# Optimization experiments

Hardware: AMD Instinct MI355X
Metric: run time of the kernel (lower is better)

The kernel has to match this reference:

```python
import jax, jax.numpy as jnp
import numpy as np

B, S, D = 1, 2048, 2048
H, KV, HD = 32, 8, 64
POWER = 100000.0


def _rotary(x):
    # x: [B, h, S, HD]; faithful to RotaryEncoder: freqs = pos / div_term
    rot_dim = HD // 2
    pos = jnp.arange(S, dtype=x.dtype)
    div = POWER ** (jnp.arange(0, HD, 2, dtype=x.dtype) / HD)  # [HD//2]
    freqs = pos[:, None] / div  # [S, HD//2]
    cos, sin = jnp.cos(freqs), jnp.sin(freqs)
    x_rot, x_pass = x[..., :rot_dim], x[..., rot_dim:]
    h = rot_dim // 2
    rot_half = jnp.concatenate([-x_rot[..., h:], x_rot[..., :h]], axis=-1)
    return jnp.concatenate([x_rot * cos + rot_half * sin, x_pass], axis=-1)


def setup_inputs() -> dict:
    key = jax.random.key(0)
    k1, k2, k3 = jax.random.split(key, 3)
    hidden_states = jax.random.normal(k1, (B, S, D), dtype=jnp.float32)
    op_size = H * HD + 2 * KV * HD
    Wqkv = jax.random.normal(k2, (D, op_size), dtype=jnp.float32) * 0.02
    Wo = jax.random.normal(k3, (H * HD, D), dtype=jnp.float32) * 0.02
    causal = jnp.tril(jnp.ones((S, S), dtype=bool))
    attention_mask = jnp.where(causal, 0.0, -1e9).astype(jnp.float32)[None, None]
    return {"hidden_states": hidden_states, "attention_mask": attention_mask,
            "Wqkv": Wqkv, "Wo": Wo}


def reference(hidden_states, attention_mask, Wqkv, Wo):
    groups = H // KV
    qkv = hidden_states @ Wqkv  # [B, S, op_size]
    qpos = H * HD
    q = qkv[..., :qpos].reshape(B, S, H, HD).transpose(0, 2, 1, 3)
    k = qkv[..., qpos:qpos + KV * HD].reshape(B, S, KV, HD).transpose(0, 2, 1, 3)
    v = qkv[..., qpos + KV * HD:].reshape(B, S, KV, HD).transpose(0, 2, 1, 3)
    q = _rotary(q)
    k = _rotary(k)
    k = jnp.repeat(k, groups, axis=1)  # GQA repeat_interleave -> [B, H, S, HD]
    v = jnp.repeat(v, groups, axis=1)
    scores = jnp.einsum('bhqd,bhkd->bhqk', q, k) / jnp.sqrt(jnp.float32(HD))
    scores = scores + attention_mask[..., :S]
    attn = jax.nn.softmax(scores.astype(jnp.float32), axis=-1).astype(v.dtype)
    out = jnp.einsum('bhqk,bhkd->bhqd', attn, v)
    out = out.transpose(0, 2, 1, 3).reshape(B, S, H * HD)
    return out @ Wo
```

## Files before the change

### kernel.cpp

```cpp
#include <hip/hip_runtime.h>
#include <hip/hip_bf16.h>
#include <cstdint>
#include <cstddef>

#define S_LEN 2048
#define D_MODEL 2048
#define NH 32
#define NKV 8
#define HDIM 64
#define OPSZ 3072
#define KOFF 2048
#define VOFF 2560

typedef float    floatx4 __attribute__((ext_vector_type(4)));
typedef __bf16   bf16x8  __attribute__((ext_vector_type(8)));
typedef __bf16   bf16x4  __attribute__((ext_vector_type(4)));
typedef __bf16   bf16_t;
typedef _Float16 f16_t;
typedef _Float16 f16x2   __attribute__((ext_vector_type(2)));
typedef _Float16 f16x4   __attribute__((ext_vector_type(4)));
typedef _Float16 f16x8   __attribute__((ext_vector_type(8)));
typedef __fp16   hfx2    __attribute__((ext_vector_type(2)));

__device__ __forceinline__ void gld16(const void* g, void* l) {
  __builtin_amdgcn_global_load_lds((__attribute__((address_space(1))) void*)(void*)g,
                                   (__attribute__((address_space(3))) void*)l,
                                   16, 0, 0);
}

__global__ __launch_bounds__(256)
void prep_kernel(const float* __restrict__ X, const float* __restrict__ Wqkv,
                 const float* __restrict__ Wo, bf16_t* __restrict__ Xb,
                 bf16_t* __restrict__ WqkvT, bf16_t* __restrict__ WoT) {
  const int bx = blockIdx.x;
  const int k0 = blockIdx.y * 32;
  const int tx = threadIdx.x & 31, ty = threadIdx.x >> 5;
  if (bx < 160) {
    __shared__ float tile[32][33];
    const float* W; bf16_t* Wt; int N, n0;
    if (bx < 96) { W = Wqkv; Wt = WqkvT; N = OPSZ;    n0 = bx * 32; }
    else         { W = Wo;   Wt = WoT;   N = D_MODEL; n0 = (bx - 96) * 32; }
#pragma unroll
    for (int i = 0; i < 32; i += 8)
      tile[ty + i][tx] = W[(size_t)(k0 + ty + i) * N + n0 + tx];
    __syncthreads();
#pragma unroll
    for (int i = 0; i < 32; i += 8)
      Wt[(size_t)(n0 + ty + i) * D_MODEL + k0 + tx] = (bf16_t)tile[tx][ty + i];
  } else {
    const int n0 = (bx - 160) * 32;
#pragma unroll
    for (int i = 0; i < 32; i += 8) {
      const size_t idx = (size_t)(k0 + ty + i) * D_MODEL + n0 + tx;
      Xb[idx] = (bf16_t)X[idx];
    }
  }
}

#define GEMM64_CORE(A_, Bt_, K_, m0_, n0_)                                        \
  const int tid = threadIdx.x;                                                    \
  const int wave = tid >> 6;                                                      \
  const int lane = tid & 63;                                                      \
  const int lane15 = lane & 15;                                                   \
  const int quad = lane >> 4;                                                     \
  const int wm = (wave & 1) * 32;                                                 \
  const int wn = (wave >> 1) * 64;                                                \
  floatx4 acc[2][4];                                                              \
  _Pragma("unroll") for (int i = 0; i < 2; i++)                                   \
    _Pragma("unroll") for (int j = 0; j < 4; j++)                                 \
      acc[i][j] = floatx4{0.f, 0.f, 0.f, 0.f};                                    \
  {                                                                               \
     \
    int arow[2], acol[2], apan[2];                                                \
    _Pragma("unroll") for (int i = 0; i < 2; i++) {                               \
      const int c = tid + i * 256;                                                \
      apan[i] = c >> 8; arow[i] = (c & 255) >> 2; acol[i] = (c & 3) * 8;          \
    }                                                                             \
                            \
    int brow[4], bcol[4], bpan[4];                                                \
    _Pragma("unroll") for (int i = 0; i < 4; i++) {                               \
      const int c = tid + i * 256;                                                \
      bpan[i] = c >> 9; brow[i] = (c & 511) >> 2; bcol[i] = (c & 3) * 8;          \
    }                                                                             \
    const bf16_t* Ab = (A_) + (size_t)(m0_) * (K_);                               \
    const bf16_t* Bb = (Bt_) + (size_t)(n0_) * (K_);                              \
    auto stage = [&](bf16_t* dA, bf16_t* dB, int k0) {                            \
      _Pragma("unroll") for (int i = 0; i < 2; i++)                               \
        gld16(Ab + (size_t)arow[i] * (K_) + k0 + apan[i] * 32 + acol[i],          \
              dA + (i * 256 + wave * 64) * 8);                                    \
      _Pragma("unroll") for (int i = 0; i < 4; i++)                               \
        gld16(Bb + (size_t)brow[i] * (K_) + k0 + bpan[i] * 32 + bcol[i],          \
              dB + (i * 256 + wave * 64) * 8);                                    \
    };                                                                            \
    auto comp = [&](const bf16_t* sA, const bf16_t* sB) {                         \
      _Pragma("unroll") for (int kt = 0; kt < 2; kt++) {                          \
        bf16x8 af[2], bfr[4];                                                     \
        _Pragma("unroll") for (int mi = 0; mi < 2; mi++)                          \
          af[mi] = *(const bf16x8*)&sA[kt * 2048 + (wm + mi * 16 + lane15) * 32 + quad * 8]; \
        _Pragma("unroll") for (int ni = 0; ni < 4; ni++)                          \
          bfr[ni] = *(const bf16x8*)&sB[kt * 4096 + (wn + ni * 16 + lane15) * 32 + quad * 8]; \
        _Pragma("unroll") for (int mi = 0; mi < 2; mi++)                          \
          _Pragma("unroll") for (int ni = 0; ni < 4; ni++)                        \
            acc[mi][ni] = __builtin_amdgcn_mfma_f32_16x16x32_bf16(af[mi], bfr[ni],\
                                                                  acc[mi][ni], 0, 0, 0); \
      }                                                                           \
    };                                                                            \
    const int NT = (K_) / 64;                           \
    stage(As0, Bs0, 0);                                                           \
    __syncthreads();                                                              \
    for (int t = 0; t < NT; t += 2) {                                             \
      stage(As1, Bs1, (t + 1) * 64);          \
      comp(As0, Bs0);                                                             \
      __syncthreads();                           \
      if (t + 2 < NT) stage(As0, Bs0, (t + 2) * 64);                              \
      comp(As1, Bs1);                                                             \
      __syncthreads();                                                            \
    }                                                                             \
  }

#define GEMM64_LDS                                                                \
  __shared__ bf16_t As0[2 * 64 * 32];                                             \
  __shared__ bf16_t As1[2 * 64 * 32];                                             \
  __shared__ bf16_t Bs0[2 * 128 * 32];                                            \
  __shared__ bf16_t Bs1[2 * 128 * 32];

#define QSCALE 0.18033688011112042f
__global__ __launch_bounds__(256, 3)
void gemm_qkv_rope(const bf16_t* __restrict__ A, const bf16_t* __restrict__ Bt,
                   bf16_t* __restrict__ Qr, bf16_t* __restrict__ Kr,
                   f16_t* __restrict__ VtG) {
  GEMM64_LDS
  const int m0 = blockIdx.y * 64;
  const int n0 = blockIdx.x * 128;
  GEMM64_CORE(A, Bt, D_MODEL, m0, n0)

  const int colbase = n0 + wn;
  const int s0 = m0 + wm;

  if (colbase < VOFF) {
    const bool isQ = (colbase < KOFF);
    const float k2 = 0.51905126483f;
    const float pj0 = exp2f(-(float)lane15 * k2);
    const float pj1 = pj0 * 0.0031622776601684f;
    bf16_t* dst = isQ ? (Qr + ((size_t)(colbase >> 6) * S_LEN) * HDIM)
                      : (Kr + ((size_t)((colbase - KOFF) >> 6) * S_LEN) * HDIM);
    const float qs = isQ ? QSCALE : 1.0f;
#pragma unroll
    for (int mi = 0; mi < 2; mi++) {
#pragma unroll
      for (int r = 0; r < 4; r++) {
        const int s = s0 + mi * 16 + quad * 4 + r;
        const float sf = (float)s;
        float s0s, s0c, s1s, s1c;
        __sincosf(sf * pj0, &s0s, &s0c);
        __sincosf(sf * pj1, &s1s, &s1c);
        const float x0 = acc[mi][0][r], x1 = acc[mi][1][r];
        bf16_t* row = dst + (size_t)s * HDIM + lane15;
        row[0]  = (bf16_t)((x0 * s0c - x1 * s0s) * qs);
        row[16] = (bf16_t)((x1 * s1c + x0 * s1s) * qs);
        row[32] = (bf16_t)(acc[mi][2][r] * qs);
        row[48] = (bf16_t)(acc[mi][3][r] * qs);
      }
    }
  } else {
    const int kvv = (colbase - VOFF) >> 6;
    f16_t* dst = VtG + (size_t)kvv * HDIM * S_LEN;
#pragma unroll
    for (int mi = 0; mi < 2; mi++) {
      const int s = s0 + mi * 16 + quad * 4;
#pragma unroll
      for (int ni = 0; ni < 4; ni++) {
        const int d = ni * 16 + lane15;
        f16x4 tv;
#pragma unroll
        for (int r = 0; r < 4; r++) tv[r] = (f16_t)acc[mi][ni][r];
        *(f16x4*)&dst[(size_t)d * S_LEN + s] = tv;
      }
    }
  }
}

__global__ __launch_bounds__(256, 3)
void gemm_bt_f32out(const bf16_t* __restrict__ A, const bf16_t* __restrict__ Bt,
                    float* __restrict__ C, int M, int N, int K) {
  GEMM64_LDS
  const int m0 = blockIdx.y * 64;
  const int n0 = blockIdx.x * 128;
  GEMM64_CORE(A, Bt, K, m0, n0)

#pragma unroll
  for (int mi = 0; mi < 2; mi++)
#pragma unroll
    for (int r = 0; r < 4; r++) {
      const int row = m0 + wm + mi * 16 + quad * 4 + r;
#pragma unroll
      for (int ni = 0; ni < 4; ni++) {
        const int col = n0 + wn + ni * 16 + lane15;
        C[(size_t)row * N + col] = acc[mi][ni][r];
      }
    }
}

__global__ __launch_bounds__(256, 4)
void flash_kernel(const bf16_t* __restrict__ Qr, const bf16_t* __restrict__ Kr,
                  const f16_t* __restrict__ VtG, bf16_t* __restrict__ attn) {
  __shared__ bf16_t Ks[128 * 64];
  __shared__ f16_t  Vt[64 * 128];

  const int tid = threadIdx.x;
  const int wave = tid >> 6;
  const int lane = tid & 63;
  const int lane15 = lane & 15;
  const int quad = lane >> 4;
  const int bx = blockIdx.x;
  const int h = bx & 31;
  const int qblk = 31 - (bx >> 5);
  const int q0 = qblk * 64;
  const int rq = q0 + wave * 16;
  const int kv = h >> 2;
  const size_t kbase = (size_t)kv * S_LEN * HDIM;
  const size_t vbase = (size_t)kv * HDIM * S_LEN;

  const int krow0 = tid >> 3;
  const int kcol  = ((((tid & 7) * 16) ^ ((krow0 & 7) << 4)) >> 1);
  const int vd0   = tid >> 4;
  const int vcol  = ((((tid & 15) * 16) ^ ((vd0 & 15) << 4)) >> 1);

  const int kswz = (lane15 & 7) << 4;
  const int vswz = lane15 << 4;

  bf16x8 aq[2];
#pragma unroll
  for (int kt = 0; kt < 2; kt++)
    aq[kt] = *(const bf16x8*)&Qr[((size_t)h * S_LEN + rq + lane15) * HDIM + kt * 32 + quad * 8];

  const f16x4 vone = {(f16_t)1.0f, (f16_t)1.0f, (f16_t)1.0f, (f16_t)1.0f};

  float m_run = -1e30f;
  floatx4 lacc = floatx4{0.f, 0.f, 0.f, 0.f};
  floatx4 o[4];
#pragma unroll
  for (int dt = 0; dt < 4; dt++) o[dt] = floatx4{0.f, 0.f, 0.f, 0.f};

  const int nk = (qblk + 2) >> 1;

  for (int t = 0; t < nk; ++t) {
    const int p0 = t * 128;
    __syncthreads();
#pragma unroll
    for (int i = 0; i < 4; i++)
      gld16(Kr + kbase + (size_t)(p0 + krow0 + i * 32) * HDIM + kcol,
            &Ks[(i * 256 + wave * 64) * 8]);
#pragma unroll
    for (int i = 0; i < 4; i++)
      gld16(VtG + vbase + (size_t)(vd0 + i * 16) * S_LEN + p0 + vcol,
            &Vt[(i * 256 + wave * 64) * 8]);
    __syncthreads();

    floatx4 sc[8];
#pragma unroll
    for (int nt = 0; nt < 8; nt++) sc[nt] = floatx4{0.f, 0.f, 0.f, 0.f};
#pragma unroll
    for (int kt = 0; kt < 2; kt++) {
#pragma unroll
      for (int nt = 0; nt < 8; nt++) {
        const bf16x8 ak = *(const bf16x8*)&Ks[(nt * 16 + lane15) * 64 +
                                              (((kt * 64 + quad * 16) ^ kswz) >> 1)];
        sc[nt] = __builtin_amdgcn_mfma_f32_16x16x32_bf16(ak, aq[kt], sc[nt], 0, 0, 0);
      }
    }

    if (p0 + 127 > rq) {
#pragma unroll
      for (int nt = 0; nt < 8; nt++)
#pragma unroll
        for (int r = 0; r < 4; r++) {
          const int kpos = p0 + nt * 16 + quad * 4 + r;
          const int qrow = rq + lane15;
          if (kpos > qrow) sc[nt][r] = -1e30f;
        }
    }

    float mt = -1e30f;
#pragma unroll
    for (int nt = 0; nt < 8; nt++) {
      mt = fmaxf(fmaxf(mt, sc[nt][0]), sc[nt][1]);
      mt = fmaxf(fmaxf(mt, sc[nt][2]), sc[nt][3]);
    }
    mt = fmaxf(mt, __shfl_xor(mt, 16));
    mt = fmaxf(mt, __shfl_xor(mt, 32));
    const float mnew = fmaxf(m_run, mt);
    const float alpha = __builtin_amdgcn_exp2f(m_run - mnew);
    m_run = mnew;

    f16x4 ph[8];
#pragma unroll
    for (int nt = 0; nt < 8; nt++) {
      const float e0 = __builtin_amdgcn_exp2f(sc[nt][0] - mnew);
      const float e1 = __builtin_amdgcn_exp2f(sc[nt][1] - mnew);
      const float e2 = __builtin_amdgcn_exp2f(sc[nt][2] - mnew);
      const float e3 = __builtin_amdgcn_exp2f(sc[nt][3] - mnew);
      const hfx2 lo_ = __builtin_amdgcn_cvt_pkrtz(e0, e1);
      const hfx2 hi_ = __builtin_amdgcn_cvt_pkrtz(e2, e3);
      const f16x2 lo = __builtin_bit_cast(f16x2, lo_);
      const f16x2 hi = __builtin_bit_cast(f16x2, hi_);
      ph[nt] = __builtin_shufflevector(lo, hi, 0, 1, 2, 3);
    }

    lacc = lacc * alpha;
#pragma unroll
    for (int dt = 0; dt < 4; dt++) o[dt] = o[dt] * alpha;

#pragma unroll
    for (int kt4 = 0; kt4 < 8; kt4++) {
      lacc = __builtin_amdgcn_mfma_f32_16x16x16f16(vone, ph[kt4], lacc, 0, 0, 0);
#pragma unroll
      for (int dt = 0; dt < 4; dt++) {
        const f16x4 av = *(const f16x4*)&Vt[(dt * 16 + lane15) * 128 +
                                            (((kt4 * 32 + quad * 8) ^ vswz) >> 1)];
        o[dt] = __builtin_amdgcn_mfma_f32_16x16x16f16(av, ph[kt4], o[dt], 0, 0, 0);
      }
    }
  }

  const float inv = 1.0f / lacc[0];
  const int s = rq + lane15;
#pragma unroll
  for (int dt = 0; dt < 4; dt++) {
    bf16x4 tv;
#pragma unroll
    for (int r = 0; r < 4; r++) tv[r] = (bf16_t)(o[dt][r] * inv);
    *(bf16x4*)&attn[(size_t)s * D_MODEL + h * HDIM + dt * 16 + quad * 4] = tv;
  }
}

extern "C" void kernel_launch(void* const* d_in, const int* in_sizes, int n_in,
                              void* d_out, int out_size, void* d_ws, size_t ws_size,
                              hipStream_t stream) {
  (void)in_sizes; (void)n_in; (void)out_size; (void)ws_size;
  const float* hidden = (const float*)d_in[0];
  const float* Wqkv = (const float*)d_in[2];
  const float* Wo   = (const float*)d_in[3];
  float* out = (float*)d_out;

  char* ws = (char*)d_ws;
  size_t off = 0;
  auto alloc = [&](size_t bytes) -> void* {
    void* p = ws + off;
    off += (bytes + 255) & ~(size_t)255;
    return p;
  };
  bf16_t* Xb    = (bf16_t*)alloc((size_t)S_LEN * D_MODEL * 2);
  bf16_t* WqkvT = (bf16_t*)alloc((size_t)OPSZ * D_MODEL * 2);
  bf16_t* WoT   = (bf16_t*)alloc((size_t)D_MODEL * D_MODEL * 2);
  bf16_t* Qr    = (bf16_t*)alloc((size_t)NH * S_LEN * HDIM * 2);
  bf16_t* Kr    = (bf16_t*)alloc((size_t)NKV * S_LEN * HDIM * 2);
  f16_t*  VtG   = (f16_t*) alloc((size_t)NKV * HDIM * S_LEN * 2);
  bf16_t* attn  = (bf16_t*)alloc((size_t)S_LEN * D_MODEL * 2);

  prep_kernel<<<dim3(224, 64), 256, 0, stream>>>(hidden, Wqkv, Wo, Xb, WqkvT, WoT);
  gemm_qkv_rope<<<dim3(OPSZ / 128, S_LEN / 64), 256, 0, stream>>>(Xb, WqkvT, Qr, Kr, VtG);
  flash_kernel<<<dim3(32 * NH), 256, 0, stream>>>(Qr, Kr, VtG, attn);
  gemm_bt_f32out<<<dim3(D_MODEL / 128, S_LEN / 64), 256, 0, stream>>>(attn, WoT, out, S_LEN, D_MODEL, D_MODEL);
}
```

Baseline: 211.6 us.

## Double-buffer K/V in flash kernel and pipeline GEMM loads with vmcnt waits

The GEMM main loop now issues two stages of global-to-LDS loads ahead and waits with partial vmcnt counts plus raw barriers instead of full __syncthreads. The flash-attention kernel gets double-buffered K and V tiles in LDS, so the next tile is prefetched while the current one is computed. The aim is to hide global load latency behind MFMA work. The cost is doubled LDS in the flash kernel, with occupancy bounds lowered from 4 to 2 blocks, and a reliance on hand-counted vmcnt values being correct.

```diff
diff --git a/kernel.cpp b/kernel.cpp
--- a/kernel.cpp
+++ b/kernel.cpp
@@ -27,6 +27,13 @@
                                    (__attribute__((address_space(3))) void*)l,
                                    16, 0, 0);
 }
+
+#define ACQ(N) do { asm volatile("s_waitcnt vmcnt(" #N ")" ::: "memory");        \
+                    __builtin_amdgcn_s_barrier();                                \
+                    __builtin_amdgcn_sched_barrier(0); } while (0)
+#define REL()  do { __builtin_amdgcn_sched_barrier(0);                           \
+                    __builtin_amdgcn_s_barrier();                                \
+                    __builtin_amdgcn_sched_barrier(0); } while (0)
 
 __global__ __launch_bounds__(256)
 void prep_kernel(const float* __restrict__ X, const float* __restrict__ Wqkv,
@@ -70,13 +77,11 @@
     _Pragma("unroll") for (int j = 0; j < 4; j++)                                 \
       acc[i][j] = floatx4{0.f, 0.f, 0.f, 0.f};                                    \
   {                                                                               \
-     \
     int arow[2], acol[2], apan[2];                                                \
     _Pragma("unroll") for (int i = 0; i < 2; i++) {                               \
       const int c = tid + i * 256;                                                \
       apan[i] = c >> 8; arow[i] = (c & 255) >> 2; acol[i] = (c & 3) * 8;          \
     }                                                                             \
-                            \
     int brow[4], bcol[4], bpan[4];                                                \
     _Pragma("unroll") for (int i = 0; i < 4; i++) {                               \
       const int c = tid + i * 256;                                                \
@@ -105,17 +110,23 @@
                                                                   acc[mi][ni], 0, 0, 0); \
       }                                                                           \
     };                                                                            \
-    const int NT = (K_) / 64;                           \
+    const int NT = (K_) / 64;                \
     stage(As0, Bs0, 0);                                                           \
-    __syncthreads();                                                              \
-    for (int t = 0; t < NT; t += 2) {                                             \
-      stage(As1, Bs1, (t + 1) * 64);          \
+    stage(As1, Bs1, 64);                                                          \
+    for (int t = 0; t < NT - 2; t += 2) {                                         \
+      ACQ(6);                                                                     \
       comp(As0, Bs0);                                                             \
-      __syncthreads();                           \
-      if (t + 2 < NT) stage(As0, Bs0, (t + 2) * 64);                              \
+      REL();                                                                      \
+      stage(As0, Bs0, (t + 2) * 64);                                              \
+      ACQ(6);                                                                     \
       comp(As1, Bs1);                                                             \
-      __syncthreads();                                                            \
+      REL();                                                                      \
+      stage(As1, Bs1, (t + 3) * 64);                                              \
     }                                                                             \
+    ACQ(6);                                                                       \
+    comp(As0, Bs0);                                                               \
+    ACQ(0);                                                                       \
+    comp(As1, Bs1);                                                               \
   }
 
 #define GEMM64_LDS                                                                \
@@ -201,11 +212,13 @@
     }
 }
 
-__global__ __launch_bounds__(256, 4)
+__global__ __launch_bounds__(256, 2)
 void flash_kernel(const bf16_t* __restrict__ Qr, const bf16_t* __restrict__ Kr,
                   const f16_t* __restrict__ VtG, bf16_t* __restrict__ attn) {
-  __shared__ bf16_t Ks[128 * 64];
-  __shared__ f16_t  Vt[64 * 128];
+  __shared__ bf16_t Ks0[128 * 64];
+  __shared__ bf16_t Ks1[128 * 64];
+  __shared__ f16_t  Vt0[64 * 128];
+  __shared__ f16_t  Vt1[64 * 128];
 
   const int tid = threadIdx.x;
   const int wave = tid >> 6;
@@ -244,18 +257,29 @@
 
   const int nk = (qblk + 2) >> 1;
 
+  auto stageKV = [&](bf16_t* kd, f16_t* vd, int p0) {
+#pragma unroll
+    for (int i = 0; i < 4; i++)
+      gld16(Kr + kbase + (size_t)(p0 + krow0 + i * 32) * HDIM + kcol,
+            kd + (i * 256 + wave * 64) * 8);
+#pragma unroll
+    for (int i = 0; i < 4; i++)
+      gld16(VtG + vbase + (size_t)(vd0 + i * 16) * S_LEN + p0 + vcol,
+            vd + (i * 256 + wave * 64) * 8);
+  };
+
+  bf16_t* ksc = Ks0; bf16_t* kso = Ks1;
+  f16_t*  vtc = Vt0; f16_t*  vto = Vt1;
+  stageKV(ksc, vtc, 0);
+
   for (int t = 0; t < nk; ++t) {
     const int p0 = t * 128;
-    __syncthreads();
-#pragma unroll
-    for (int i = 0; i < 4; i++)
-      gld16(Kr + kbase + (size_t)(p0 + krow0 + i * 32) * HDIM + kcol,
-            &Ks[(i * 256 + wave * 64) * 8]);
-#pragma unroll
-    for (int i = 0; i < 4; i++)
-      gld16(VtG + vbase + (size_t)(vd0 + i * 16) * S_LEN + p0 + vcol,
-            &Vt[(i * 256 + wave * 64) * 8]);
-    __syncthreads();
+    if (t + 1 < nk) {
+      stageKV(kso, vto, (t + 1) * 128);
+      ACQ(8);
+    } else {
+      ACQ(0);
+    }
 
     floatx4 sc[8];
 #pragma unroll
@@ -264,8 +288,8 @@
     for (int kt = 0; kt < 2; kt++) {
 #pragma unroll
       for (int nt = 0; nt < 8; nt++) {
-        const bf16x8 ak = *(const bf16x8*)&Ks[(nt * 16 + lane15) * 64 +
-                                              (((kt * 64 + quad * 16) ^ kswz) >> 1)];
+        const bf16x8 ak = *(const bf16x8*)&ksc[(nt * 16 + lane15) * 64 +
+                                               (((kt * 64 + quad * 16) ^ kswz) >> 1)];
         sc[nt] = __builtin_amdgcn_mfma_f32_16x16x32_bf16(ak, aq[kt], sc[nt], 0, 0, 0);
       }
     }
@@ -316,11 +340,16 @@
       lacc = __builtin_amdgcn_mfma_f32_16x16x16f16(vone, ph[kt4], lacc, 0, 0, 0);
 #pragma unroll
       for (int dt = 0; dt < 4; dt++) {
-        const f16x4 av = *(const f16x4*)&Vt[(dt * 16 + lane15) * 128 +
-                                            (((kt4 * 32 + quad * 8) ^ vswz) >> 1)];
+        const f16x4 av = *(const f16x4*)&vtc[(dt * 16 + lane15) * 128 +
+                                             (((kt4 * 32 + quad * 8) ^ vswz) >> 1)];
         o[dt] = __builtin_amdgcn_mfma_f32_16x16x16f16(av, ph[kt4], o[dt], 0, 0, 0);
       }
     }
+
+    REL();
+
+    bf16_t* kt_ = ksc; ksc = kso; kso = kt_;
+    f16_t*  vt_ = vtc; vtc = vto; vto = vt_;
   }
 
   const float inv = 1.0f / lacc[0];
```

After: 211.0 us. No clear change (-0.3%).
